# Performance work log

Measured on AMD Instinct MI355X. Metric: run time of the kernel, lower is better.

The kernel has to match this reference:

```python
import jax, jax.numpy as jnp
import numpy as np
import math

B, S, D, H = 2, 2048, 1024, 16
HD = D // H  # 64


def setup_inputs() -> dict:
    key = jax.random.key(0)
    ks = jax.random.split(key, 7)
    scale = 1.0 / math.sqrt(D)
    return {
        "hidden_states": jax.random.normal(ks[0], (B, S, D), jnp.float32),
        "attention_mask": jnp.zeros((B, 1, 1, S), jnp.int32),  # 0 = valid (code negates .bool())
        "Wq": jax.random.normal(ks[1], (D, D), jnp.float32) * scale,
        "bq": jnp.zeros((D,), jnp.float32),
        "Wk": jax.random.normal(ks[2], (D, D), jnp.float32) * scale,
        "bk": jnp.zeros((D,), jnp.float32),
        "Wv": jax.random.normal(ks[3], (D, D), jnp.float32) * scale,
        "bv": jnp.zeros((D,), jnp.float32),
    }


def reference(hidden_states, attention_mask, Wq, bq, Wk, bk, Wv, bv):
    b, s, d = hidden_states.shape

    def proj(W, bias):
        # torch Linear: x @ W.T + b ; weight shape [out, in]
        y = jnp.einsum('bsd,ed->bse', hidden_states, W) + bias
        return y.reshape(b, s, H, HD).transpose(0, 2, 1, 3)  # b h s d

    q, k, v = proj(Wq, bq), proj(Wk, bk), proj(Wv, bv)

    scores = jnp.einsum('bhqd,bhkd->bhqk', q, k) * (1.0 / math.sqrt(HD))
    causal = jnp.tril(jnp.ones((s, s), bool))[None, None]          # [1,1,S,S]
    pad = ~(attention_mask.astype(bool))                           # [B,1,1,S], True = valid
    mask = causal & pad
    scores = jnp.where(mask, scores, -jnp.inf)
    probs = jax.nn.softmax(scores, axis=-1)  # dropout prob = 0.0 -> identity
    out = jnp.einsum('bhqk,bhkd->bhqd', probs, v)
    return out.transpose(0, 2, 1, 3).reshape(b, s, d)
```

## Files before the change

kernel.cpp:

```cpp
#include <hip/hip_runtime.h>

typedef __bf16 bf16;
typedef __bf16 bf16x4 __attribute__((ext_vector_type(4)));
typedef __bf16 bf16x8 __attribute__((ext_vector_type(8)));
typedef float f32x4 __attribute__((ext_vector_type(4)));

#define DEV __device__ __forceinline__

typedef const __attribute__((address_space(1))) void gvoid_t;
typedef __attribute__((address_space(3))) void lvoid_t;

DEV void gload_lds16(const void* g, void* l) {
  __builtin_amdgcn_global_load_lds((gvoid_t*)g, (lvoid_t*)l, 16, 0, 0);
}

DEV f32x4 mfma16(bf16x8 a, bf16x8 b, f32x4 c) {
  return __builtin_amdgcn_mfma_f32_16x16x32_bf16(a, b, c, 0, 0, 0);
}

#define QSCALE 0.18033688011112042f

__global__ __launch_bounds__(256) void cvt_all(
    const float* __restrict__ hs, const float* __restrict__ Wq,
    const float* __restrict__ Wk, const float* __restrict__ Wv,
    bf16* __restrict__ Xb, bf16* __restrict__ Wb) {
  const int i = blockIdx.x * 256 + threadIdx.x;
  const float* src;
  bf16* dst;
  int off;
  if (i < 1048576) {
    src = hs; dst = Xb; off = i;
  } else {
    const int j = i - 1048576;
    const int sel = j >> 18;
    off = j & 262143;
    src = (sel == 0) ? Wq : (sel == 1) ? Wk : Wv;
    dst = Wb + (size_t)sel * 1048576;
  }
  float4 f = reinterpret_cast<const float4*>(src)[off];
  bf16x4 o;
  o[0] = (bf16)f.x; o[1] = (bf16)f.y; o[2] = (bf16)f.z; o[3] = (bf16)f.w;
  reinterpret_cast<bf16x4*>(dst)[off] = o;
}

__global__ __launch_bounds__(256) void gemm_qkv(
    const bf16* __restrict__ X, const bf16* __restrict__ W,
    const float* __restrict__ bq, const float* __restrict__ bk,
    const float* __restrict__ bv,
    bf16* __restrict__ Q, bf16* __restrict__ Kb, bf16* __restrict__ Vt) {
  __shared__ bf16 As[128 * 64];
  __shared__ bf16 Bs[128 * 64];
  const int t = threadIdx.x;
  const int lane = t & 63, w = t >> 6;
  const int wr = w >> 1, wc = w & 1;
  const int bid = blockIdx.x;
  const int swz = (bid & 7) * 96 + (bid >> 3);
  const int m0 = (swz / 24) * 128;
  const int n0 = (swz % 24) * 128;
  const int cl = lane & 15, g8 = (lane >> 4) * 8;

  f32x4 acc[4][4];
  for (int mi = 0; mi < 4; ++mi)
    for (int ni = 0; ni < 4; ++ni)
      for (int r = 0; r < 4; ++r) acc[mi][ni][r] = 0.0f;

  for (int k0 = 0; k0 < 1024; k0 += 64) {
#pragma unroll
    for (int i = 0; i < 4; ++i) {
      int c = i * 256 + t;
      int row = c >> 3, col8 = (c & 7) * 8;
      gload_lds16(X + (size_t)(m0 + row) * 1024 + k0 + col8, As + c * 8);
      gload_lds16(W + (size_t)(n0 + row) * 1024 + k0 + col8, Bs + c * 8);
    }
    __syncthreads();
#pragma unroll
    for (int kk = 0; kk < 64; kk += 32) {
      bf16x8 a[4], b[4];
#pragma unroll
      for (int mi = 0; mi < 4; ++mi)
        a[mi] = *(const bf16x8*)&As[(wr * 64 + mi * 16 + cl) * 64 + kk + g8];
#pragma unroll
      for (int ni = 0; ni < 4; ++ni)
        b[ni] = *(const bf16x8*)&Bs[(wc * 64 + ni * 16 + cl) * 64 + kk + g8];
      __builtin_amdgcn_s_setprio(1);
#pragma unroll
      for (int mi = 0; mi < 4; ++mi)
#pragma unroll
        for (int ni = 0; ni < 4; ++ni)
          acc[mi][ni] = mfma16(a[mi], b[ni], acc[mi][ni]);
      __builtin_amdgcn_s_setprio(0);
    }
    __syncthreads();
  }

  const int rq = (lane >> 4) * 4;
#pragma unroll
  for (int mi = 0; mi < 4; ++mi) {
#pragma unroll
    for (int ni = 0; ni < 4; ++ni) {
      const int n = n0 + wc * 64 + ni * 16 + cl;
      const int mbase = m0 + wr * 64 + mi * 16 + rq;
      const int b = mbase >> 11, s0 = mbase & 2047;
      if (n < 1024) {
        const float bias = bq[n];
        const int h = n >> 6, hd = n & 63;
#pragma unroll
        for (int r = 0; r < 4; ++r)
          Q[(((size_t)(b * 16 + h)) * 2048 + s0 + r) * 64 + hd] =
              (bf16)((acc[mi][ni][r] + bias) * QSCALE);
      } else if (n < 2048) {
        const int n2 = n - 1024;
        const float bias = bk[n2];
        const int h = n2 >> 6, hd = n2 & 63;
#pragma unroll
        for (int r = 0; r < 4; ++r)
          Kb[(((size_t)(b * 16 + h)) * 2048 + s0 + r) * 64 + hd] =
              (bf16)(acc[mi][ni][r] + bias);
      } else {
        const int n2 = n - 2048;
        const float bias = bv[n2];
        const int h = n2 >> 6, hd = n2 & 63;
        bf16x4 pk;
#pragma unroll
        for (int r = 0; r < 4; ++r) pk[r] = (bf16)(acc[mi][ni][r] + bias);
        *(bf16x4*)&Vt[(((size_t)(b * 16 + h)) * 64 + hd) * 2048 + s0] = pk;
      }
    }
  }
}

__global__ __launch_bounds__(512) void flash_attn(
    const bf16* __restrict__ Q, const bf16* __restrict__ K,
    const bf16* __restrict__ Vt, const int* __restrict__ amask,
    float* __restrict__ out) {
  __shared__ bf16 Ks[2][64 * 64];
  __shared__ bf16 Vs[2][64 * 64];
  __shared__ bf16 Ps[8][16 * 64];
  __shared__ unsigned long long mk[32];
  const int t = threadIdx.x, lane = t & 63, w = t >> 6;
  const int bh = blockIdx.x & 31;
  const int p = blockIdx.x >> 5;
  const int qt = (w < 4) ? (31 - p) : p;
  const int b = bh >> 4, h = bh & 15;
  const int cl = lane & 15, g8 = (lane >> 4) * 8, rq = (lane >> 4) * 4;
  const int row0 = qt * 64 + (w & 3) * 16;
  const int ntiles = 32 - p;

  const bf16* Qp = Q + (size_t)bh * 2048 * 64;
  const bf16* Kp = K + (size_t)bh * 2048 * 64;
  const bf16* Vp = Vt + (size_t)bh * 64 * 2048;

  bf16x8 qf[2];
#pragma unroll
  for (int ks = 0; ks < 2; ++ks)
    qf[ks] = *(const bf16x8*)&Qp[(size_t)(row0 + cl) * 64 + ks * 32 + g8];

  bf16x8 ones;
#pragma unroll
  for (int j = 0; j < 8; ++j) ones[j] = (cl == 0) ? (bf16)1.0f : (bf16)0.0f;

  f32x4 o[5];
#pragma unroll
  for (int nc = 0; nc < 5; ++nc)
#pragma unroll
    for (int r = 0; r < 4; ++r) o[nc][r] = 0.0f;

#pragma unroll
  for (int i = 0; i < 4; ++i) {
    const int kt = w * 4 + i;
    const unsigned long long bal =
        __ballot(amask[b * 2048 + kt * 64 + lane] != 0);
    if (lane == 0) mk[kt] = bal;
  }
  {
    const int row = t >> 3, sl8 = ((t & 7) ^ (row & 7)) * 8;
    gload_lds16(Kp + (size_t)row * 64 + sl8, &Ks[0][t * 8]);
    gload_lds16(Vp + (size_t)row * 2048 + sl8, &Vs[0][t * 8]);
  }
  __syncthreads();

  int buf = 0;
  for (int kt = 0; kt < ntiles; ++kt) {
    const int kv0 = kt * 64;
    if (kt + 1 < ntiles) {
      const int row = t >> 3, sl8 = ((t & 7) ^ (row & 7)) * 8;
      gload_lds16(Kp + (size_t)(kv0 + 64 + row) * 64 + sl8, &Ks[buf ^ 1][t * 8]);
      gload_lds16(Vp + (size_t)row * 2048 + kv0 + 64 + sl8, &Vs[buf ^ 1][t * 8]);
    }
    if (kt <= qt) {
      const unsigned long long padb = mk[kt];
      f32x4 s4[4];
#pragma unroll
      for (int nj = 0; nj < 4; ++nj)
#pragma unroll
        for (int r = 0; r < 4; ++r) s4[nj][r] = -12.0f;
      __builtin_amdgcn_s_setprio(1);
#pragma unroll
      for (int ks = 0; ks < 2; ++ks) {
#pragma unroll
        for (int nj = 0; nj < 4; ++nj) {
          const int row = nj * 16 + cl;
          const bf16x8 kf = *(const bf16x8*)&Ks[buf][row * 64 +
                                ((ks * 32 + g8) ^ ((row & 7) << 3))];
          s4[nj] = mfma16(qf[ks], kf, s4[nj]);
        }
      }
      __builtin_amdgcn_s_setprio(0);
      const bool needm = (kt == qt) || (padb != 0ull);
#pragma unroll
      for (int nj = 0; nj < 4; ++nj)
#pragma unroll
        for (int r = 0; r < 4; ++r) {
          float x = s4[nj][r];
          if (needm) {
            const int col = kv0 + nj * 16 + cl;
            const int rowq = row0 + rq + r;
            const bool bad = (col > rowq) || ((padb >> (nj * 16 + cl)) & 1ull);
            x = bad ? -1e30f : x;
          }
          const float pv = __builtin_amdgcn_exp2f(x);
          const int rr = rq + r;
          Ps[w][rr * 64 + ((nj * 16 + cl) ^ ((rr & 7) << 3))] = (bf16)pv;
        }
      __builtin_amdgcn_s_setprio(1);
#pragma unroll
      for (int ks = 0; ks < 2; ++ks) {
        const bf16x8 pa = *(const bf16x8*)&Ps[w][cl * 64 +
                              ((ks * 32 + g8) ^ ((cl & 7) << 3))];
#pragma unroll
        for (int nc = 0; nc < 4; ++nc) {
          const int row = nc * 16 + cl;
          const bf16x8 vf = *(const bf16x8*)&Vs[buf][row * 64 +
                                ((ks * 32 + g8) ^ ((row & 7) << 3))];
          o[nc] = mfma16(pa, vf, o[nc]);
        }
        o[4] = mfma16(pa, ones, o[4]);
      }
      __builtin_amdgcn_s_setprio(0);
    }
    __syncthreads();
    buf ^= 1;
  }

#pragma unroll
  for (int r = 0; r < 4; ++r) {
    const float l = __shfl(o[4][r], lane & 48, 64);
    const float inv = 1.0f / l;
    const int rowg = row0 + rq + r;
    float* op = &out[((size_t)b * 2048 + rowg) * 1024 + h * 64];
#pragma unroll
    for (int nc = 0; nc < 4; ++nc) op[nc * 16 + cl] = o[nc][r] * inv;
  }
}

extern "C" void kernel_launch(void* const* d_in, const int* in_sizes, int n_in,
                              void* d_out, int out_size, void* d_ws,
                              size_t ws_size, hipStream_t stream) {
  const float* hs = (const float*)d_in[0];
  const int* amask = (const int*)d_in[1];
  const float* Wq = (const float*)d_in[2];
  const float* bq = (const float*)d_in[3];
  const float* Wk = (const float*)d_in[4];
  const float* bk = (const float*)d_in[5];
  const float* Wv = (const float*)d_in[6];
  const float* bv = (const float*)d_in[7];
  float* out = (float*)d_out;

  char* ws = (char*)d_ws;
  bf16* Xb = (bf16*)ws;
  bf16* Wb = (bf16*)(ws + 8ull * 1024 * 1024);
  bf16* Qb = (bf16*)(ws + 14ull * 1024 * 1024);
  bf16* Kb = (bf16*)(ws + 22ull * 1024 * 1024);
  bf16* Vtb = (bf16*)(ws + 30ull * 1024 * 1024);

  cvt_all<<<7168, 256, 0, stream>>>(hs, Wq, Wk, Wv, Xb, Wb);
  gemm_qkv<<<768, 256, 0, stream>>>(Xb, Wb, bq, bk, bv, Qb, Kb, Vtb);
  flash_attn<<<512, 512, 0, stream>>>(Qb, Kb, Vtb, amask, out);
}
```

Baseline: 89.66 us.

## Software-pipeline QK and PV across KV tiles with triple-buffered V

Restructures the flash-attention loop so each iteration's QK^T and exp for tile kt overlap with the PV MMA for tile kt-1. This uses double-buffered P tiles per warp and a triple-buffered V in LDS. The pad-mask ballot is now computed inline per tile instead of being precomputed into shared memory. The aim is to hide the softmax/exp latency behind tensor-core work, at the cost of more LDS, extra branches and a drain step after the loop.

```diff
diff --git a/kernel.cpp b/kernel.cpp
--- a/kernel.cpp
+++ b/kernel.cpp
@@ -134,9 +134,8 @@
     const bf16* __restrict__ Vt, const int* __restrict__ amask,
     float* __restrict__ out) {
   __shared__ bf16 Ks[2][64 * 64];
-  __shared__ bf16 Vs[2][64 * 64];
-  __shared__ bf16 Ps[8][16 * 64];
-  __shared__ unsigned long long mk[32];
+  __shared__ bf16 Vs[3][64 * 64];
+  __shared__ bf16 Ps[8][2][16 * 64];
   const int t = threadIdx.x, lane = t & 63, w = t >> 6;
   const int bh = blockIdx.x & 31;
   const int p = blockIdx.x >> 5;
@@ -165,13 +164,24 @@
 #pragma unroll
     for (int r = 0; r < 4; ++r) o[nc][r] = 0.0f;
 
-#pragma unroll
-  for (int i = 0; i < 4; ++i) {
-    const int kt = w * 4 + i;
-    const unsigned long long bal =
-        __ballot(amask[b * 2048 + kt * 64 + lane] != 0);
-    if (lane == 0) mk[kt] = bal;
-  }
+  auto PV = [&](int psl, int vsl) {
+    __builtin_amdgcn_s_setprio(1);
+#pragma unroll
+    for (int ks = 0; ks < 2; ++ks) {
+      const bf16x8 pa = *(const bf16x8*)&Ps[w][psl][cl * 64 +
+                            ((ks * 32 + g8) ^ ((cl & 7) << 3))];
+#pragma unroll
+      for (int nc = 0; nc < 4; ++nc) {
+        const int row = nc * 16 + cl;
+        const bf16x8 vf = *(const bf16x8*)&Vs[vsl][row * 64 +
+                              ((ks * 32 + g8) ^ ((row & 7) << 3))];
+        o[nc] = mfma16(pa, vf, o[nc]);
+      }
+      o[4] = mfma16(pa, ones, o[4]);
+    }
+    __builtin_amdgcn_s_setprio(0);
+  };
+
   {
     const int row = t >> 3, sl8 = ((t & 7) ^ (row & 7)) * 8;
     gload_lds16(Kp + (size_t)row * 64 + sl8, &Ks[0][t * 8]);
@@ -179,16 +189,21 @@
   }
   __syncthreads();
 
-  int buf = 0;
+  int v1 = 1;
   for (int kt = 0; kt < ntiles; ++kt) {
     const int kv0 = kt * 64;
     if (kt + 1 < ntiles) {
       const int row = t >> 3, sl8 = ((t & 7) ^ (row & 7)) * 8;
-      gload_lds16(Kp + (size_t)(kv0 + 64 + row) * 64 + sl8, &Ks[buf ^ 1][t * 8]);
-      gload_lds16(Vp + (size_t)row * 2048 + kv0 + 64 + sl8, &Vs[buf ^ 1][t * 8]);
-    }
-    if (kt <= qt) {
-      const unsigned long long padb = mk[kt];
+      gload_lds16(Kp + (size_t)(kv0 + 64 + row) * 64 + sl8,
+                  &Ks[(kt + 1) & 1][t * 8]);
+      gload_lds16(Vp + (size_t)row * 2048 + kv0 + 64 + sl8, &Vs[v1][t * 8]);
+    }
+    const int vm1 = (v1 + 1) % 3;
+    const bool doQK = (kt <= qt);
+    const bool doPV = (kt >= 1) & (kt <= qt + 1);
+    if (doQK & doPV) {
+      const unsigned long long padb =
+          __ballot(amask[b * 2048 + kv0 + lane] != 0);
       f32x4 s4[4];
 #pragma unroll
       for (int nj = 0; nj < 4; ++nj)
@@ -200,12 +215,13 @@
 #pragma unroll
         for (int nj = 0; nj < 4; ++nj) {
           const int row = nj * 16 + cl;
-          const bf16x8 kf = *(const bf16x8*)&Ks[buf][row * 64 +
+          const bf16x8 kf = *(const bf16x8*)&Ks[kt & 1][row * 64 +
                                 ((ks * 32 + g8) ^ ((row & 7) << 3))];
           s4[nj] = mfma16(qf[ks], kf, s4[nj]);
         }
       }
       __builtin_amdgcn_s_setprio(0);
+      PV((kt & 1) ^ 1, vm1);
       const bool needm = (kt == qt) || (padb != 0ull);
 #pragma unroll
       for (int nj = 0; nj < 4; ++nj)
@@ -220,26 +236,55 @@
           }
           const float pv = __builtin_amdgcn_exp2f(x);
           const int rr = rq + r;
-          Ps[w][rr * 64 + ((nj * 16 + cl) ^ ((rr & 7) << 3))] = (bf16)pv;
+          Ps[w][kt & 1][rr * 64 + ((nj * 16 + cl) ^ ((rr & 7) << 3))] =
+              (bf16)pv;
         }
+    } else if (doQK) {
+      const unsigned long long padb =
+          __ballot(amask[b * 2048 + kv0 + lane] != 0);
+      f32x4 s4[4];
+#pragma unroll
+      for (int nj = 0; nj < 4; ++nj)
+#pragma unroll
+        for (int r = 0; r < 4; ++r) s4[nj][r] = -12.0f;
       __builtin_amdgcn_s_setprio(1);
 #pragma unroll
       for (int ks = 0; ks < 2; ++ks) {
-        const bf16x8 pa = *(const bf16x8*)&Ps[w][cl * 64 +
-                              ((ks * 32 + g8) ^ ((cl & 7) << 3))];
-#pragma unroll
-        for (int nc = 0; nc < 4; ++nc) {
-          const int row = nc * 16 + cl;
-          const bf16x8 vf = *(const bf16x8*)&Vs[buf][row * 64 +
+#pragma unroll
+        for (int nj = 0; nj < 4; ++nj) {
+          const int row = nj * 16 + cl;
+          const bf16x8 kf = *(const bf16x8*)&Ks[kt & 1][row * 64 +
                                 ((ks * 32 + g8) ^ ((row & 7) << 3))];
-          o[nc] = mfma16(pa, vf, o[nc]);
+          s4[nj] = mfma16(qf[ks], kf, s4[nj]);
         }
-        o[4] = mfma16(pa, ones, o[4]);
       }
       __builtin_amdgcn_s_setprio(0);
+      const bool needm = (kt == qt) || (padb != 0ull);
+#pragma unroll
+      for (int nj = 0; nj < 4; ++nj)
+#pragma unroll
+        for (int r = 0; r < 4; ++r) {
+          float x = s4[nj][r];
+          if (needm) {
+            const int col = kv0 + nj * 16 + cl;
+            const int rowq = row0 + rq + r;
+            const bool bad = (col > rowq) || ((padb >> (nj * 16 + cl)) & 1ull);
+            x = bad ? -1e30f : x;
+          }
+          const float pv = __builtin_amdgcn_exp2f(x);
+          const int rr = rq + r;
+          Ps[w][kt & 1][rr * 64 + ((nj * 16 + cl) ^ ((rr & 7) << 3))] =
+              (bf16)pv;
+        }
+    } else if (doPV) {
+      PV((kt & 1) ^ 1, vm1);
     }
     __syncthreads();
-    buf ^= 1;
+    v1 = (v1 + 1) % 3;
+  }
+
+  if (w < 4) {
+    PV(qt & 1, (v1 + 1) % 3);
   }
 
 #pragma unroll
```

Measured after the change: 94.99 us. 1.06x slower.
